# Optimization experiments

Hardware: AMD Instinct MI355X
Metric: run time of the kernel (lower is better)

Reference implementation:

```python
import jax, jax.numpy as jnp
import numpy as np

N_USERS = 100000
N_ITEMS = 50000
N = N_USERS + N_ITEMS
EMB_DIM = 64
N_LAYERS = 3
NNZ = 6400000
BATCH = 4096


def setup_inputs() -> dict:
    key = jax.random.key(0)
    k = jax.random.split(key, 7)
    user_emb = 0.1 * jax.random.normal(k[0], (N_USERS, EMB_DIM), dtype=jnp.float32)
    item_emb = 0.1 * jax.random.normal(k[1], (N_ITEMS, EMB_DIM), dtype=jnp.float32)
    graph_val = jax.random.uniform(k[2], (NNZ,), dtype=jnp.float32) * 0.05
    graph_src = jax.random.randint(k[3], (NNZ,), 0, N, dtype=jnp.int64) if jax.config.jax_enable_x64 else jax.random.randint(k[3], (NNZ,), 0, N).astype(jnp.int32)
    graph_dst = jax.random.randint(k[4], (NNZ,), 0, N).astype(graph_src.dtype)
    users = jax.random.randint(k[5], (BATCH,), 0, N_USERS).astype(graph_src.dtype)
    items = jax.random.randint(k[6], (BATCH,), 0, N_ITEMS).astype(graph_src.dtype)
    return {"user_emb": user_emb, "item_emb": item_emb, "graph_val": graph_val,
            "graph_src": graph_src, "graph_dst": graph_dst, "users": users, "items": items}


def _spmm(val, src, dst, x):
    # y[src] += val * x[dst]  -- sparse (COO) matrix @ dense
    return jax.ops.segment_sum(val[:, None] * x[dst], src, num_segments=N)


def reference(user_emb, item_emb, graph_val, graph_src, graph_dst, users, items):
    all_emb = jnp.concatenate([user_emb, item_emb], axis=0)  # [N, d]
    acc = all_emb  # running sum over layers (fused mean accumulation)
    x = all_emb
    for _ in range(N_LAYERS):
        x = _spmm(graph_val, graph_src, graph_dst, x)
        acc = acc + x
    light_out = acc / (N_LAYERS + 1)
    all_users = light_out[:N_USERS]
    all_items = light_out[N_USERS:]
    scores = jnp.sum(all_users[users] * all_items[items], axis=1)  # [B]
    return scores
```

## Files before the change

### kernel.cpp

```cpp
#include <hip/hip_runtime.h>


constexpr int N_USERS = 100000;
constexpr int N_ITEMS = 50000;
constexpr int N_NODES = N_USERS + N_ITEMS;
constexpr int EMB = 64;
constexpr int NNZ = 6400000;
constexpr int BATCH = 4096;

constexpr int BSHIFT = 9;
constexpr int BWIDTH = 1 << BSHIFT;
constexpr int NB = (N_NODES + BWIDTH - 1) >> BSHIFT;
constexpr int NBPAD = 512;
constexpr int BSTRIDE = 23500;
constexpr int PBSTRIDE = 26624;

constexpr int TILE = 5120;
constexpr int P1_BLOCKS = NNZ / TILE;
constexpr int EPT1 = TILE / 256;

constexpr float QSCALE = 327680.0f;
constexpr float QINV   = 1.0f / 327680.0f;

__global__ void gcur_init_kernel(int* __restrict__ gcur) {
    int i = blockIdx.x * blockDim.x + threadIdx.x;
    if (i < NB) gcur[i] = i * BSTRIDE;
}

__global__ void p1_bin_kernel(const int* __restrict__ src, const int* __restrict__ dst,
                              const float* __restrict__ val, int* __restrict__ gcur,
                              uint2* __restrict__ staging) {
    __shared__ int hist[NBPAD];
    __shared__ int gbase[NBPAD];
    __shared__ int cur[NBPAD];
    __shared__ int sbuf[NBPAD];
    __shared__ int lbase[NBPAD];
    __shared__ uint2 ebuf[TILE];
    int t = threadIdx.x;
    int tile = blockIdx.x * TILE;
    int srcs[EPT1];
    #pragma unroll
    for (int k = 0; k < EPT1; ++k) srcs[k] = src[tile + t + k * 256];
    for (int i = t; i < NBPAD; i += 256) { hist[i] = 0; cur[i] = 0; }
    __syncthreads();
    #pragma unroll
    for (int k = 0; k < EPT1; ++k) atomicAdd(&hist[srcs[k] >> BSHIFT], 1);
    __syncthreads();
    for (int i = t; i < NB; i += 256) {
        int h = hist[i];
        gbase[i] = (h > 0) ? atomicAdd(&gcur[i], h) : 0;
    }
    for (int i = t; i < NBPAD; i += 256) sbuf[i] = hist[i];
    __syncthreads();
    int* pin = sbuf; int* pout = lbase;
    for (int off = 1; off < NBPAD; off <<= 1) {
        for (int i = t; i < NBPAD; i += 256) {
            int v = pin[i];
            if (i >= off) v += pin[i - off];
            pout[i] = v;
        }
        __syncthreads();
        int* tmp = pin; pin = pout; pout = tmp;
    }
    for (int i = t; i < NBPAD; i += 256) lbase[i] = pin[i] - hist[i];
    __syncthreads();
    #pragma unroll
    for (int k = 0; k < EPT1; ++k) {
        int i = tile + t + k * 256;
        int s = srcs[k];
        int b = s >> BSHIFT;
        int c = atomicAdd(&cur[b], 1);
        int d = dst[i];
        float v = val[i];
        unsigned q = (unsigned)(v * QSCALE);
        if (q > 16383u) q = 16383u;
        ebuf[lbase[b] + c] = make_uint2((q << 18) | (unsigned)d, (unsigned)s);
    }
    __syncthreads();
    #pragma unroll
    for (int k = 0; k < EPT1; ++k) {
        int j = t + k * 256;
        uint2 e = ebuf[j];
        int b = (int)(e.y >> BSHIFT);
        unsigned pos = (unsigned)(gbase[b] + (j - lbase[b]));
        if (pos < (unsigned)((b + 1) * BSTRIDE))
            staging[pos] = e;
    }
}

__global__ void p2_sort_kernel(const int* __restrict__ gcur, const uint2* __restrict__ staging,
                               unsigned* __restrict__ epack, unsigned* __restrict__ prow) {
    __shared__ int hist[BWIDTH], sA[BWIDTH], sB[BWIDTH], cur[BWIDTH];
    int b = blockIdx.x;
    int t = threadIdx.x;
    int cnt = gcur[b] - b * BSTRIDE;
    if (cnt > BSTRIDE) cnt = BSTRIDE;
    int sbase = b * BSTRIDE;
    hist[t] = 0;
    __syncthreads();
    for (int j = t; j < cnt; j += 512) {
        uint2 e = staging[sbase + j];
        atomicAdd(&hist[e.y & (BWIDTH - 1)], 1);
    }
    __syncthreads();
    sA[t] = (hist[t] + 7) >> 3;
    __syncthreads();
    int* pin = sA; int* pout = sB;
    for (int off = 1; off < BWIDTH; off <<= 1) {
        int v = pin[t];
        if (t >= off) v += pin[t - off];
        pout[t] = v;
        __syncthreads();
        int* tmp = pin; pin = pout; pout = tmp;
    }
    {
        int c = hist[t];
        int pw = (c + 7) >> 3;
        int ps = pin[t] - pw;
        unsigned poff = (unsigned)(b * PBSTRIDE + 8 * ps);
        int fit = (PBSTRIDE - 8 * ps) >> 3;
        if (fit < 0) fit = 0;
        if (pw > fit) pw = fit;
        if (pw > 15) pw = 15;
        cur[t] = (int)poff;
        int node = (b << BSHIFT) + t;
        if (node < N_NODES) prow[node] = (poff << 4) | (unsigned)pw;
        for (int s = c; s < 8 * pw; ++s) epack[poff + s] = 0;
    }
    __syncthreads();
    unsigned bend = (unsigned)((b + 1) * PBSTRIDE);
    for (int j = t; j < cnt; j += 512) {
        uint2 e = staging[sbase + j];
        int p = atomicAdd(&cur[e.y & (BWIDTH - 1)], 1);
        if ((unsigned)p < bend) epack[p] = e.x;
    }
}

__device__ __forceinline__ float ubf0(unsigned x) { return (float)(x & 0xffu); }
__device__ __forceinline__ float ubf1(unsigned x) { return (float)((x >> 8) & 0xffu); }
__device__ __forceinline__ float ubf2(unsigned x) { return (float)((x >> 16) & 0xffu); }
__device__ __forceinline__ float ubf3(unsigned x) { return (float)(x >> 24); }

__global__ void initq_kernel(const float* __restrict__ ue, const float* __restrict__ ie,
                             unsigned char* __restrict__ x8, float* __restrict__ scl) {
    int gid = blockIdx.x * blockDim.x + threadIdx.x;
    int row = gid >> 3;
    if (row >= N_NODES) return;
    int l8 = threadIdx.x & 7;
    const float* srcp = (row < N_USERS) ? (ue + (size_t)row * EMB)
                                        : (ie + (size_t)(row - N_USERS) * EMB);
    const float4* p = (const float4*)(srcp + l8 * 8);
    float4 f0 = p[0], f1 = p[1];
    float v[8] = {f0.x, f0.y, f0.z, f0.w, f1.x, f1.y, f1.z, f1.w};
    float m = 0.f;
    #pragma unroll
    for (int k = 0; k < 8; ++k) m = fmaxf(m, fabsf(v[k]));
    m = fmaxf(m, __shfl_xor(m, 1, 64));
    m = fmaxf(m, __shfl_xor(m, 2, 64));
    m = fmaxf(m, __shfl_xor(m, 4, 64));
    float inv = (m > 0.f) ? 127.f / m : 0.f;
    unsigned w0 = 0, w1 = 0;
    #pragma unroll
    for (int k = 0; k < 4; ++k)
        w0 |= (((unsigned)((int)rintf(v[k] * inv) + 128)) & 0xffu) << (8 * k);
    #pragma unroll
    for (int k = 0; k < 4; ++k)
        w1 |= (((unsigned)((int)rintf(v[4 + k] * inv) + 128)) & 0xffu) << (8 * k);
    *(uint2*)(x8 + (((size_t)row) << 6) + l8 * 8) = make_uint2(w0, w1);
    if (l8 == 0) scl[row] = m * (1.f / 127.f);
}

__global__ void gather_init_kernel(const float* __restrict__ ue, const float* __restrict__ ie,
                                   const int* __restrict__ users, const int* __restrict__ items,
                                   float* __restrict__ accb) {
    int gid = blockIdx.x * blockDim.x + threadIdx.x;
    int w = gid >> 6;
    int lane = threadIdx.x & 63;
    if (w >= BATCH * 2) return;
    int b = w >> 1;
    float v;
    if (w & 1) v = ie[(long long)items[b] * EMB + lane];
    else       v = ue[(long long)users[b] * EMB + lane];
    accb[(long long)w * EMB + lane] = v;
}

__global__ void gather_addq_kernel(const unsigned char* __restrict__ x8,
                                   const float* __restrict__ scl,
                                   const int* __restrict__ users, const int* __restrict__ items,
                                   float* __restrict__ accb) {
    int gid = blockIdx.x * blockDim.x + threadIdx.x;
    int w = gid >> 6;
    int lane = threadIdx.x & 63;
    if (w >= BATCH * 2) return;
    int b = w >> 1;
    int node = (w & 1) ? (N_USERS + items[b]) : users[b];
    float s = scl[node];
    float xv = s * ((float)x8[(((size_t)node) << 6) + lane] - 128.f);
    accb[(long long)w * EMB + lane] += xv;
}

__device__ __forceinline__ void row_gather_q8(unsigned pr, int lane,
                                              const unsigned* __restrict__ epack,
                                              const unsigned char* __restrict__ x8,
                                              const float* __restrict__ scl,
                                              float acc[8]) {
    const int l8 = lane & 7;
    const int qb = lane & 56;
    const unsigned li8 = (unsigned)l8 * 8u;
    float a0 = 0, a1 = 0, a2 = 0, a3 = 0, a4 = 0, a5 = 0, a6 = 0, a7 = 0;
    float b0 = 0, b1 = 0, b2 = 0, b3 = 0, b4 = 0, b5 = 0, b6 = 0, b7 = 0;
    float S = 0.f;
    const unsigned* ep = epack + (pr >> 4);
    int nwin = (int)(pr & 15u);
    if (nwin > 0) {
        unsigned e = ep[l8];
        for (int w = 0; w < nwin; ++w) {
            unsigned en = ep[8 + l8];
            ep += 8;
            unsigned d = e & 0x3FFFFu;
            float v = ((float)(e >> 18) + 0.5f) * QINV;
            float vs = v * scl[d];
            unsigned voff = d << 6;
            #pragma unroll
            for (int t = 0; t < 8; t += 2) {
                unsigned offA = (unsigned)__shfl((int)voff, qb + t, 64);
                unsigned offB = (unsigned)__shfl((int)voff, qb + t + 1, 64);
                float vA = __shfl(vs, qb + t, 64);
                float vB = __shfl(vs, qb + t + 1, 64);
                uint2 pa = *(const uint2*)(x8 + (offA | li8));
                uint2 pb = *(const uint2*)(x8 + (offB | li8));
                a0 += vA * ubf0(pa.x);  a1 += vA * ubf1(pa.x);
                a2 += vA * ubf2(pa.x);  a3 += vA * ubf3(pa.x);
                a4 += vA * ubf0(pa.y);  a5 += vA * ubf1(pa.y);
                a6 += vA * ubf2(pa.y);  a7 += vA * ubf3(pa.y);
                b0 += vB * ubf0(pb.x);  b1 += vB * ubf1(pb.x);
                b2 += vB * ubf2(pb.x);  b3 += vB * ubf3(pb.x);
                b4 += vB * ubf0(pb.y);  b5 += vB * ubf1(pb.y);
                b6 += vB * ubf2(pb.y);  b7 += vB * ubf3(pb.y);
                S += vA + vB;
            }
            e = en;
        }
    }
    float c = 128.f * S;
    acc[0] = a0 + b0 - c; acc[1] = a1 + b1 - c; acc[2] = a2 + b2 - c;
    acc[3] = a3 + b3 - c; acc[4] = a4 + b4 - c; acc[5] = a5 + b5 - c;
    acc[6] = a6 + b6 - c; acc[7] = a7 + b7 - c;
}

__global__ void spmmq_kernel(const unsigned* __restrict__ prow,
                             const unsigned* __restrict__ epack,
                             const unsigned char* __restrict__ x8,
                             const float* __restrict__ sclin,
                             unsigned char* __restrict__ y8,
                             float* __restrict__ sclout) {
    int gid = blockIdx.x * blockDim.x + threadIdx.x;
    int row = gid >> 3;
    if (row >= N_NODES) return;
    int lane = threadIdx.x & 63;
    float acc[8];
    row_gather_q8(prow[row], lane, epack, x8, sclin, acc);
    float m = 0.f;
    #pragma unroll
    for (int k = 0; k < 8; ++k) m = fmaxf(m, fabsf(acc[k]));
    m = fmaxf(m, __shfl_xor(m, 1, 64));
    m = fmaxf(m, __shfl_xor(m, 2, 64));
    m = fmaxf(m, __shfl_xor(m, 4, 64));
    float inv = (m > 0.f) ? 127.f / m : 0.f;
    unsigned w0 = 0, w1 = 0;
    #pragma unroll
    for (int k = 0; k < 4; ++k)
        w0 |= (((unsigned)((int)rintf(acc[k] * inv) + 128)) & 0xffu) << (8 * k);
    #pragma unroll
    for (int k = 0; k < 4; ++k)
        w1 |= (((unsigned)((int)rintf(acc[4 + k] * inv) + 128)) & 0xffu) << (8 * k);
    int l8 = lane & 7;
    *(uint2*)(y8 + (((size_t)row) << 6) + l8 * 8) = make_uint2(w0, w1);
    if (l8 == 0) sclout[row] = m * (1.f / 127.f);
}

__global__ void spmm_selq_kernel(const unsigned* __restrict__ prow,
                                 const unsigned* __restrict__ epack,
                                 const unsigned char* __restrict__ x8,
                                 const float* __restrict__ scl,
                                 const int* __restrict__ users, const int* __restrict__ items,
                                 float* __restrict__ accb) {
    int gid = blockIdx.x * blockDim.x + threadIdx.x;
    int g = gid >> 3;
    if (g >= BATCH * 2) return;
    int lane = threadIdx.x & 63;
    int b = g >> 1;
    int node = (g & 1) ? (N_USERS + items[b]) : users[b];
    float acc[8];
    row_gather_q8(prow[node], lane, epack, x8, scl, acc);
    float4* p = (float4*)(accb + ((long long)g << 6) + (lane & 7) * 8);
    float4 c0 = p[0], c1 = p[1];
    c0.x += acc[0]; c0.y += acc[1]; c0.z += acc[2]; c0.w += acc[3];
    c1.x += acc[4]; c1.y += acc[5]; c1.z += acc[6]; c1.w += acc[7];
    p[0] = c0; p[1] = c1;
}

__global__ void score_kernel(const float* __restrict__ accb, float* __restrict__ out) {
    int gid = blockIdx.x * blockDim.x + threadIdx.x;
    int b = gid >> 6;
    int lane = threadIdx.x & 63;
    if (b >= BATCH) return;
    float a = accb[(long long)(2 * b) * EMB + lane];
    float c = accb[(long long)(2 * b + 1) * EMB + lane];
    float p = a * c;
    #pragma unroll
    for (int off = 32; off > 0; off >>= 1) p += __shfl_down(p, off, 64);
    if (lane == 0) out[b] = p * (1.0f / 16.0f);
}

extern "C" void kernel_launch(void* const* d_in, const int* in_sizes, int n_in,
                              void* d_out, int out_size, void* d_ws, size_t ws_size,
                              hipStream_t stream) {
    const float* user_emb  = (const float*)d_in[0];
    const float* item_emb  = (const float*)d_in[1];
    const float* graph_val = (const float*)d_in[2];
    const int*   graph_src = (const int*)d_in[3];
    const int*   graph_dst = (const int*)d_in[4];
    const int*   users     = (const int*)d_in[5];
    const int*   items     = (const int*)d_in[6];
    float* out = (float*)d_out;

    char* base = (char*)d_ws;
    const size_t STAGE_BYTES = (size_t)BSTRIDE * NB * 8;
    const size_t XQBYTES = (size_t)N_NODES * 64;
    const size_t ACCB_BYTES = (size_t)BATCH * 2 * EMB * 4;
    const size_t PB_SLOTS = (size_t)PBSTRIDE * NB;
    uint2*         staging = (uint2*)base;
    unsigned char* A8      = (unsigned char*)base;
    unsigned char* B8      = A8 + XQBYTES;
    float*         accb    = (float*)(base + 2 * XQBYTES);
    float*         scA     = (float*)(base + 2 * XQBYTES + ACCB_BYTES);
    float*         scB     = scA + N_NODES;
    unsigned*      epack   = (unsigned*)(base + STAGE_BYTES);
    unsigned*      prow    = epack + PB_SLOTS;
    int*           gcur    = (int*)(prow + N_NODES);

    const int wblocks = (BATCH * 2 * 64) / 256;
    const int sblocks = (N_NODES * 8 + 255) / 256;
    const int selblocks = (BATCH * 2 * 8) / 256;

    gcur_init_kernel<<<(NB + 255) / 256, 256, 0, stream>>>(gcur);
    p1_bin_kernel<<<P1_BLOCKS, 256, 0, stream>>>(graph_src, graph_dst, graph_val,
                                                 gcur, staging);
    p2_sort_kernel<<<NB, 512, 0, stream>>>(gcur, staging, epack, prow);

    initq_kernel<<<sblocks, 256, 0, stream>>>(user_emb, item_emb, A8, scA);
    gather_init_kernel<<<wblocks, 256, 0, stream>>>(user_emb, item_emb, users, items, accb);

    spmmq_kernel<<<sblocks, 256, 0, stream>>>(prow, epack, A8, scA, B8, scB);
    gather_addq_kernel<<<wblocks, 256, 0, stream>>>(B8, scB, users, items, accb);

    spmmq_kernel<<<sblocks, 256, 0, stream>>>(prow, epack, B8, scB, A8, scA);
    gather_addq_kernel<<<wblocks, 256, 0, stream>>>(A8, scA, users, items, accb);

    spmm_selq_kernel<<<selblocks, 256, 0, stream>>>(prow, epack, A8, scA, users, items, accb);

    score_kernel<<<(BATCH * 64) / 256, 256, 0, stream>>>(accb, out);
}
```

Measured before the change: 489.3 us.

## Horizontally fuse build, quantize and gather kernels; add nontemporal memory hints

Merges edge binning, initial int8 quantization and the batch gather-init into one launch using block-index ranges. Each gather-add is folded into the following SpMM launch, and the last gather-add is merged with the selective final SpMM, using atomics on the batch accumulator. The sort kernel now runs 1024 threads per block, and nontemporal loads and stores are applied to streaming edge and embedding traffic. The workspace layout is reorganised so that staging aliases the second quantized buffer. Together these cut launch count and let independent work overlap, at the cost of atomics and more complex kernels.

Result: slower. 603.4 us (+23.3%).

```diff
diff --git a/kernel.cpp b/kernel.cpp
--- a/kernel.cpp
+++ b/kernel.cpp
@@ -18,73 +18,140 @@
 constexpr int TILE = 5120;
 constexpr int P1_BLOCKS = NNZ / TILE;
 constexpr int EPT1 = TILE / 256;
+constexpr int IQ_BLOCKS = (N_NODES * 8 + 255) / 256;
+constexpr int GI_BLOCKS = (BATCH * 2 * 64) / 256;
+constexpr int SBLOCKS  = (N_NODES * 8 + 255) / 256;
+constexpr int SELBLOCKS = (BATCH * 2 * 8) / 256;
 
 constexpr float QSCALE = 327680.0f;
 constexpr float QINV   = 1.0f / 327680.0f;
+
+__device__ __forceinline__ unsigned ntl_u32(const unsigned* p) { return __builtin_nontemporal_load(p); }
+__device__ __forceinline__ int      ntl_i32(const int* p)      { return __builtin_nontemporal_load(p); }
+__device__ __forceinline__ float    ntl_f32(const float* p)    { return __builtin_nontemporal_load(p); }
+__device__ __forceinline__ unsigned long long ntl_u64(const unsigned long long* p) { return __builtin_nontemporal_load(p); }
+__device__ __forceinline__ void nts_u32(unsigned v, unsigned* p) { __builtin_nontemporal_store(v, p); }
+__device__ __forceinline__ void nts_u64(unsigned long long v, unsigned long long* p) { __builtin_nontemporal_store(v, p); }
 
 __global__ void gcur_init_kernel(int* __restrict__ gcur) {
     int i = blockIdx.x * blockDim.x + threadIdx.x;
     if (i < NB) gcur[i] = i * BSTRIDE;
 }
 
-__global__ void p1_bin_kernel(const int* __restrict__ src, const int* __restrict__ dst,
-                              const float* __restrict__ val, int* __restrict__ gcur,
-                              uint2* __restrict__ staging) {
-    __shared__ int hist[NBPAD];
-    __shared__ int gbase[NBPAD];
-    __shared__ int cur[NBPAD];
-    __shared__ int sbuf[NBPAD];
-    __shared__ int lbase[NBPAD];
-    __shared__ uint2 ebuf[TILE];
+__device__ __forceinline__ float ubf0(unsigned x) { return (float)(x & 0xffu); }
+__device__ __forceinline__ float ubf1(unsigned x) { return (float)((x >> 8) & 0xffu); }
+__device__ __forceinline__ float ubf2(unsigned x) { return (float)((x >> 16) & 0xffu); }
+__device__ __forceinline__ float ubf3(unsigned x) { return (float)(x >> 24); }
+
+__global__ void fused_build_kernel(const int* __restrict__ src, const int* __restrict__ dst,
+                                   const float* __restrict__ val, int* __restrict__ gcur,
+                                   uint2* __restrict__ staging,
+                                   const float* __restrict__ ue, const float* __restrict__ ie,
+                                   const int* __restrict__ users, const int* __restrict__ items,
+                                   unsigned char* __restrict__ x8, float* __restrict__ scl,
+                                   float* __restrict__ accb) {
+    int bx = blockIdx.x;
     int t = threadIdx.x;
-    int tile = blockIdx.x * TILE;
-    int srcs[EPT1];
-    #pragma unroll
-    for (int k = 0; k < EPT1; ++k) srcs[k] = src[tile + t + k * 256];
-    for (int i = t; i < NBPAD; i += 256) { hist[i] = 0; cur[i] = 0; }
-    __syncthreads();
-    #pragma unroll
-    for (int k = 0; k < EPT1; ++k) atomicAdd(&hist[srcs[k] >> BSHIFT], 1);
-    __syncthreads();
-    for (int i = t; i < NB; i += 256) {
-        int h = hist[i];
-        gbase[i] = (h > 0) ? atomicAdd(&gcur[i], h) : 0;
-    }
-    for (int i = t; i < NBPAD; i += 256) sbuf[i] = hist[i];
-    __syncthreads();
-    int* pin = sbuf; int* pout = lbase;
-    for (int off = 1; off < NBPAD; off <<= 1) {
-        for (int i = t; i < NBPAD; i += 256) {
-            int v = pin[i];
-            if (i >= off) v += pin[i - off];
-            pout[i] = v;
-        }
-        __syncthreads();
-        int* tmp = pin; pin = pout; pout = tmp;
-    }
-    for (int i = t; i < NBPAD; i += 256) lbase[i] = pin[i] - hist[i];
-    __syncthreads();
-    #pragma unroll
-    for (int k = 0; k < EPT1; ++k) {
-        int i = tile + t + k * 256;
-        int s = srcs[k];
-        int b = s >> BSHIFT;
-        int c = atomicAdd(&cur[b], 1);
-        int d = dst[i];
-        float v = val[i];
-        unsigned q = (unsigned)(v * QSCALE);
-        if (q > 16383u) q = 16383u;
-        ebuf[lbase[b] + c] = make_uint2((q << 18) | (unsigned)d, (unsigned)s);
-    }
-    __syncthreads();
-    #pragma unroll
-    for (int k = 0; k < EPT1; ++k) {
-        int j = t + k * 256;
-        uint2 e = ebuf[j];
-        int b = (int)(e.y >> BSHIFT);
-        unsigned pos = (unsigned)(gbase[b] + (j - lbase[b]));
-        if (pos < (unsigned)((b + 1) * BSTRIDE))
-            staging[pos] = e;
+    if (bx < P1_BLOCKS) {
+        __shared__ int hist[NBPAD];
+        __shared__ int gbase[NBPAD];
+        __shared__ int cur[NBPAD];
+        __shared__ int sbuf[NBPAD];
+        __shared__ int lbase[NBPAD];
+        __shared__ uint2 ebuf[TILE];
+        int tile = bx * TILE;
+        int srcs[EPT1];
+        #pragma unroll
+        for (int k = 0; k < EPT1; ++k) srcs[k] = ntl_i32(src + tile + t + k * 256);
+        for (int i = t; i < NBPAD; i += 256) { hist[i] = 0; cur[i] = 0; }
+        __syncthreads();
+        #pragma unroll
+        for (int k = 0; k < EPT1; ++k) atomicAdd(&hist[srcs[k] >> BSHIFT], 1);
+        __syncthreads();
+        for (int i = t; i < NB; i += 256) {
+            int h = hist[i];
+            gbase[i] = (h > 0) ? atomicAdd(&gcur[i], h) : 0;
+        }
+        for (int i = t; i < NBPAD; i += 256) sbuf[i] = hist[i];
+        __syncthreads();
+        int* pin = sbuf; int* pout = lbase;
+        for (int off = 1; off < NBPAD; off <<= 1) {
+            for (int i = t; i < NBPAD; i += 256) {
+                int v = pin[i];
+                if (i >= off) v += pin[i - off];
+                pout[i] = v;
+            }
+            __syncthreads();
+            int* tmp = pin; pin = pout; pout = tmp;
+        }
+        for (int i = t; i < NBPAD; i += 256) lbase[i] = pin[i] - hist[i];
+        __syncthreads();
+        #pragma unroll
+        for (int k = 0; k < EPT1; ++k) {
+            int i = tile + t + k * 256;
+            int s = srcs[k];
+            int b = s >> BSHIFT;
+            int c = atomicAdd(&cur[b], 1);
+            int d = ntl_i32(dst + i);
+            float v = ntl_f32(val + i);
+            unsigned q = (unsigned)(v * QSCALE);
+            if (q > 16383u) q = 16383u;
+            ebuf[lbase[b] + c] = make_uint2((q << 18) | (unsigned)d, (unsigned)s);
+        }
+        __syncthreads();
+        #pragma unroll
+        for (int k = 0; k < EPT1; ++k) {
+            int j = t + k * 256;
+            uint2 e = ebuf[j];
+            int b = (int)(e.y >> BSHIFT);
+            unsigned pos = (unsigned)(gbase[b] + (j - lbase[b]));
+            if (pos < (unsigned)((b + 1) * BSTRIDE))
+                nts_u64(((unsigned long long)e.y << 32) | (unsigned long long)e.x,
+                        (unsigned long long*)&staging[pos]);
+        }
+        return;
+    }
+    bx -= P1_BLOCKS;
+    if (bx < IQ_BLOCKS) {
+        int gid = bx * 256 + t;
+        int row = gid >> 3;
+        if (row >= N_NODES) return;
+        int l8 = t & 7;
+        const float* srcp = (row < N_USERS) ? (ue + (size_t)row * EMB)
+                                            : (ie + (size_t)(row - N_USERS) * EMB);
+        const float4* p = (const float4*)(srcp + l8 * 8);
+        float4 f0 = p[0], f1 = p[1];
+        float v[8] = {f0.x, f0.y, f0.z, f0.w, f1.x, f1.y, f1.z, f1.w};
+        float m = 0.f;
+        #pragma unroll
+        for (int k = 0; k < 8; ++k) m = fmaxf(m, fabsf(v[k]));
+        m = fmaxf(m, __shfl_xor(m, 1, 64));
+        m = fmaxf(m, __shfl_xor(m, 2, 64));
+        m = fmaxf(m, __shfl_xor(m, 4, 64));
+        float inv = (m > 0.f) ? 127.f / m : 0.f;
+        unsigned w0 = 0, w1 = 0;
+        #pragma unroll
+        for (int k = 0; k < 4; ++k)
+            w0 |= (((unsigned)((int)rintf(v[k] * inv) + 128)) & 0xffu) << (8 * k);
+        #pragma unroll
+        for (int k = 0; k < 4; ++k)
+            w1 |= (((unsigned)((int)rintf(v[4 + k] * inv) + 128)) & 0xffu) << (8 * k);
+        nts_u64(((unsigned long long)w1 << 32) | (unsigned long long)w0,
+                (unsigned long long*)(x8 + (((size_t)row) << 6) + l8 * 8));
+        if (l8 == 0) scl[row] = m * (1.f / 127.f);
+        return;
+    }
+    bx -= IQ_BLOCKS;
+    {
+        int gid = bx * 256 + t;
+        int w = gid >> 6;
+        int lane = t & 63;
+        if (w >= BATCH * 2) return;
+        int b = w >> 1;
+        float v;
+        if (w & 1) v = ie[(long long)items[b] * EMB + lane];
+        else       v = ue[(long long)users[b] * EMB + lane];
+        accb[(long long)w * EMB + lane] = v;
     }
 }
 
@@ -95,25 +162,28 @@
     int t = threadIdx.x;
     int cnt = gcur[b] - b * BSTRIDE;
     if (cnt > BSTRIDE) cnt = BSTRIDE;
+    if (cnt < 0) cnt = 0;
     int sbase = b * BSTRIDE;
-    hist[t] = 0;
+    if (t < BWIDTH) hist[t] = 0;
     __syncthreads();
-    for (int j = t; j < cnt; j += 512) {
+    for (int j = t; j < cnt; j += 1024) {
         uint2 e = staging[sbase + j];
         atomicAdd(&hist[e.y & (BWIDTH - 1)], 1);
     }
     __syncthreads();
-    sA[t] = (hist[t] + 7) >> 3;
+    if (t < BWIDTH) sA[t] = (hist[t] + 7) >> 3;
     __syncthreads();
     int* pin = sA; int* pout = sB;
     for (int off = 1; off < BWIDTH; off <<= 1) {
-        int v = pin[t];
-        if (t >= off) v += pin[t - off];
-        pout[t] = v;
+        if (t < BWIDTH) {
+            int v = pin[t];
+            if (t >= off) v += pin[t - off];
+            pout[t] = v;
+        }
         __syncthreads();
         int* tmp = pin; pin = pout; pout = tmp;
     }
-    {
+    if (t < BWIDTH) {
         int c = hist[t];
         int pw = (c + 7) >> 3;
         int ps = pin[t] - pw;
@@ -129,74 +199,13 @@
     }
     __syncthreads();
     unsigned bend = (unsigned)((b + 1) * PBSTRIDE);
-    for (int j = t; j < cnt; j += 512) {
-        uint2 e = staging[sbase + j];
-        int p = atomicAdd(&cur[e.y & (BWIDTH - 1)], 1);
-        if ((unsigned)p < bend) epack[p] = e.x;
-    }
-}
-
-__device__ __forceinline__ float ubf0(unsigned x) { return (float)(x & 0xffu); }
-__device__ __forceinline__ float ubf1(unsigned x) { return (float)((x >> 8) & 0xffu); }
-__device__ __forceinline__ float ubf2(unsigned x) { return (float)((x >> 16) & 0xffu); }
-__device__ __forceinline__ float ubf3(unsigned x) { return (float)(x >> 24); }
-
-__global__ void initq_kernel(const float* __restrict__ ue, const float* __restrict__ ie,
-                             unsigned char* __restrict__ x8, float* __restrict__ scl) {
-    int gid = blockIdx.x * blockDim.x + threadIdx.x;
-    int row = gid >> 3;
-    if (row >= N_NODES) return;
-    int l8 = threadIdx.x & 7;
-    const float* srcp = (row < N_USERS) ? (ue + (size_t)row * EMB)
-                                        : (ie + (size_t)(row - N_USERS) * EMB);
-    const float4* p = (const float4*)(srcp + l8 * 8);
-    float4 f0 = p[0], f1 = p[1];
-    float v[8] = {f0.x, f0.y, f0.z, f0.w, f1.x, f1.y, f1.z, f1.w};
-    float m = 0.f;
-    #pragma unroll
-    for (int k = 0; k < 8; ++k) m = fmaxf(m, fabsf(v[k]));
-    m = fmaxf(m, __shfl_xor(m, 1, 64));
-    m = fmaxf(m, __shfl_xor(m, 2, 64));
-    m = fmaxf(m, __shfl_xor(m, 4, 64));
-    float inv = (m > 0.f) ? 127.f / m : 0.f;
-    unsigned w0 = 0, w1 = 0;
-    #pragma unroll
-    for (int k = 0; k < 4; ++k)
-        w0 |= (((unsigned)((int)rintf(v[k] * inv) + 128)) & 0xffu) << (8 * k);
-    #pragma unroll
-    for (int k = 0; k < 4; ++k)
-        w1 |= (((unsigned)((int)rintf(v[4 + k] * inv) + 128)) & 0xffu) << (8 * k);
-    *(uint2*)(x8 + (((size_t)row) << 6) + l8 * 8) = make_uint2(w0, w1);
-    if (l8 == 0) scl[row] = m * (1.f / 127.f);
-}
-
-__global__ void gather_init_kernel(const float* __restrict__ ue, const float* __restrict__ ie,
-                                   const int* __restrict__ users, const int* __restrict__ items,
-                                   float* __restrict__ accb) {
-    int gid = blockIdx.x * blockDim.x + threadIdx.x;
-    int w = gid >> 6;
-    int lane = threadIdx.x & 63;
-    if (w >= BATCH * 2) return;
-    int b = w >> 1;
-    float v;
-    if (w & 1) v = ie[(long long)items[b] * EMB + lane];
-    else       v = ue[(long long)users[b] * EMB + lane];
-    accb[(long long)w * EMB + lane] = v;
-}
-
-__global__ void gather_addq_kernel(const unsigned char* __restrict__ x8,
-                                   const float* __restrict__ scl,
-                                   const int* __restrict__ users, const int* __restrict__ items,
-                                   float* __restrict__ accb) {
-    int gid = blockIdx.x * blockDim.x + threadIdx.x;
-    int w = gid >> 6;
-    int lane = threadIdx.x & 63;
-    if (w >= BATCH * 2) return;
-    int b = w >> 1;
-    int node = (w & 1) ? (N_USERS + items[b]) : users[b];
-    float s = scl[node];
-    float xv = s * ((float)x8[(((size_t)node) << 6) + lane] - 128.f);
-    accb[(long long)w * EMB + lane] += xv;
+    for (int j = t; j < cnt; j += 1024) {
+        unsigned long long ev = ntl_u64((const unsigned long long*)&staging[sbase + j]);
+        unsigned ex = (unsigned)ev;
+        int row = (int)((ev >> 32) & (unsigned long long)(BWIDTH - 1));
+        int p = atomicAdd(&cur[row], 1);
+        if ((unsigned)p < bend) nts_u32(ex, &epack[p]);
+    }
 }
 
 __device__ __forceinline__ void row_gather_q8(unsigned pr, int lane,
@@ -213,9 +222,9 @@
     const unsigned* ep = epack + (pr >> 4);
     int nwin = (int)(pr & 15u);
     if (nwin > 0) {
-        unsigned e = ep[l8];
+        unsigned e = ntl_u32(ep + l8);
         for (int w = 0; w < nwin; ++w) {
-            unsigned en = ep[8 + l8];
+            unsigned en = ntl_u32(ep + 8 + l8);
             ep += 8;
             unsigned d = e & 0x3FFFFu;
             float v = ((float)(e >> 18) + 0.5f) * QINV;
@@ -248,56 +257,93 @@
     acc[6] = a6 + b6 - c; acc[7] = a7 + b7 - c;
 }
 
-__global__ void spmmq_kernel(const unsigned* __restrict__ prow,
-                             const unsigned* __restrict__ epack,
-                             const unsigned char* __restrict__ x8,
-                             const float* __restrict__ sclin,
-                             unsigned char* __restrict__ y8,
-                             float* __restrict__ sclout) {
-    int gid = blockIdx.x * blockDim.x + threadIdx.x;
-    int row = gid >> 3;
-    if (row >= N_NODES) return;
-    int lane = threadIdx.x & 63;
-    float acc[8];
-    row_gather_q8(prow[row], lane, epack, x8, sclin, acc);
-    float m = 0.f;
-    #pragma unroll
-    for (int k = 0; k < 8; ++k) m = fmaxf(m, fabsf(acc[k]));
-    m = fmaxf(m, __shfl_xor(m, 1, 64));
-    m = fmaxf(m, __shfl_xor(m, 2, 64));
-    m = fmaxf(m, __shfl_xor(m, 4, 64));
-    float inv = (m > 0.f) ? 127.f / m : 0.f;
-    unsigned w0 = 0, w1 = 0;
-    #pragma unroll
-    for (int k = 0; k < 4; ++k)
-        w0 |= (((unsigned)((int)rintf(acc[k] * inv) + 128)) & 0xffu) << (8 * k);
-    #pragma unroll
-    for (int k = 0; k < 4; ++k)
-        w1 |= (((unsigned)((int)rintf(acc[4 + k] * inv) + 128)) & 0xffu) << (8 * k);
-    int l8 = lane & 7;
-    *(uint2*)(y8 + (((size_t)row) << 6) + l8 * 8) = make_uint2(w0, w1);
-    if (l8 == 0) sclout[row] = m * (1.f / 127.f);
-}
-
-__global__ void spmm_selq_kernel(const unsigned* __restrict__ prow,
-                                 const unsigned* __restrict__ epack,
-                                 const unsigned char* __restrict__ x8,
-                                 const float* __restrict__ scl,
-                                 const int* __restrict__ users, const int* __restrict__ items,
-                                 float* __restrict__ accb) {
-    int gid = blockIdx.x * blockDim.x + threadIdx.x;
-    int g = gid >> 3;
-    if (g >= BATCH * 2) return;
-    int lane = threadIdx.x & 63;
-    int b = g >> 1;
-    int node = (g & 1) ? (N_USERS + items[b]) : users[b];
-    float acc[8];
-    row_gather_q8(prow[node], lane, epack, x8, scl, acc);
-    float4* p = (float4*)(accb + ((long long)g << 6) + (lane & 7) * 8);
-    float4 c0 = p[0], c1 = p[1];
-    c0.x += acc[0]; c0.y += acc[1]; c0.z += acc[2]; c0.w += acc[3];
-    c1.x += acc[4]; c1.y += acc[5]; c1.z += acc[6]; c1.w += acc[7];
-    p[0] = c0; p[1] = c1;
+__global__ void spmmq_fused_kernel(const unsigned* __restrict__ prow,
+                                   const unsigned* __restrict__ epack,
+                                   const unsigned char* __restrict__ x8in,
+                                   const float* __restrict__ sclin,
+                                   unsigned char* __restrict__ y8,
+                                   float* __restrict__ sclout,
+                                   const int* __restrict__ users,
+                                   const int* __restrict__ items,
+                                   float* __restrict__ accb) {
+    int bx = blockIdx.x;
+    int t = threadIdx.x;
+    if (bx < SBLOCKS) {
+        int gid = bx * 256 + t;
+        int row = gid >> 3;
+        if (row >= N_NODES) return;
+        int lane = t & 63;
+        unsigned pr = ntl_u32(prow + row);
+        float acc[8];
+        row_gather_q8(pr, lane, epack, x8in, sclin, acc);
+        float m = 0.f;
+        #pragma unroll
+        for (int k = 0; k < 8; ++k) m = fmaxf(m, fabsf(acc[k]));
+        m = fmaxf(m, __shfl_xor(m, 1, 64));
+        m = fmaxf(m, __shfl_xor(m, 2, 64));
+        m = fmaxf(m, __shfl_xor(m, 4, 64));
+        float inv = (m > 0.f) ? 127.f / m : 0.f;
+        unsigned w0 = 0, w1 = 0;
+        #pragma unroll
+        for (int k = 0; k < 4; ++k)
+            w0 |= (((unsigned)((int)rintf(acc[k] * inv) + 128)) & 0xffu) << (8 * k);
+        #pragma unroll
+        for (int k = 0; k < 4; ++k)
+            w1 |= (((unsigned)((int)rintf(acc[4 + k] * inv) + 128)) & 0xffu) << (8 * k);
+        int l8 = lane & 7;
+        nts_u64(((unsigned long long)w1 << 32) | (unsigned long long)w0,
+                (unsigned long long*)(y8 + (((size_t)row) << 6) + l8 * 8));
+        if (l8 == 0) sclout[row] = m * (1.f / 127.f);
+        return;
+    }
+    bx -= SBLOCKS;
+    {
+        int gid = bx * 256 + t;
+        int w = gid >> 6;
+        int lane = t & 63;
+        if (w >= BATCH * 2) return;
+        int b = w >> 1;
+        int node = (w & 1) ? (N_USERS + items[b]) : users[b];
+        float s = sclin[node];
+        float xv = s * ((float)x8in[(((size_t)node) << 6) + lane] - 128.f);
+        accb[(long long)w * EMB + lane] += xv;
+    }
+}
+
+__global__ void tail_kernel(const unsigned* __restrict__ prow,
+                            const unsigned* __restrict__ epack,
+                            const unsigned char* __restrict__ x8,
+                            const float* __restrict__ scl,
+                            const int* __restrict__ users, const int* __restrict__ items,
+                            float* __restrict__ accb) {
+    int bx = blockIdx.x;
+    int t = threadIdx.x;
+    if (bx < GI_BLOCKS) {
+        int gid = bx * 256 + t;
+        int w = gid >> 6;
+        int lane = t & 63;
+        if (w >= BATCH * 2) return;
+        int b = w >> 1;
+        int node = (w & 1) ? (N_USERS + items[b]) : users[b];
+        float s = scl[node];
+        float xv = s * ((float)x8[(((size_t)node) << 6) + lane] - 128.f);
+        atomicAdd(&accb[(long long)w * EMB + lane], xv);
+        return;
+    }
+    bx -= GI_BLOCKS;
+    {
+        int gid = bx * 256 + t;
+        int g = gid >> 3;
+        if (g >= BATCH * 2) return;
+        int lane = t & 63;
+        int b = g >> 1;
+        int node = (g & 1) ? (N_USERS + items[b]) : users[b];
+        float acc[8];
+        row_gather_q8(ntl_u32(prow + node), lane, epack, x8, scl, acc);
+        float* p = accb + ((long long)g << 6) + (lane & 7) * 8;
+        #pragma unroll
+        for (int k = 0; k < 8; ++k) atomicAdd(p + k, acc[k]);
+    }
 }
 
 __global__ void score_kernel(const float* __restrict__ accb, float* __restrict__ out) {
@@ -340,25 +386,36 @@
     unsigned*      prow    = epack + PB_SLOTS;
     int*           gcur    = (int*)(prow + N_NODES);
 
-    const int wblocks = (BATCH * 2 * 64) / 256;
-    const int sblocks = (N_NODES * 8 + 255) / 256;
-    const int selblocks = (BATCH * 2 * 8) / 256;
+    const size_t X_REGION = 2 * XQBYTES + ACCB_BYTES + 2 * (size_t)N_NODES * 4;
+    const size_t X_REGION_AL = (X_REGION + 255) & ~(size_t)255;
+    staging = (uint2*)(base + X_REGION_AL);
+    epack   = (unsigned*)(base + X_REGION_AL + STAGE_BYTES);
+    prow    = epack + PB_SLOTS;
+    gcur    = (int*)(prow + N_NODES);
+    accb = (float*)(gcur + 512);
+    scA  = accb + (size_t)BATCH * 2 * EMB;
+    scB  = scA + N_NODES;
+    A8   = (unsigned char*)base;
+    B8   = A8 + XQBYTES;
+    staging = (uint2*)(base + XQBYTES);
+    epack   = (unsigned*)(base + XQBYTES + STAGE_BYTES);
+    prow    = epack + PB_SLOTS;
+    gcur    = (int*)(prow + N_NODES);
+    accb    = (float*)(gcur + 512);
+    scA     = accb + (size_t)BATCH * 2 * EMB;
+    scB     = scA + N_NODES;
 
     gcur_init_kernel<<<(NB + 255) / 256, 256, 0, stream>>>(gcur);
-    p1_bin_kernel<<<P1_BLOCKS, 256, 0, stream>>>(graph_src, graph_dst, graph_val,
-                                                 gcur, staging);
-    p2_sort_kernel<<<NB, 512, 0, stream>>>(gcur, staging, epack, prow);
-
-    initq_kernel<<<sblocks, 256, 0, stream>>>(user_emb, item_emb, A8, scA);
-    gather_init_kernel<<<wblocks, 256, 0, stream>>>(user_emb, item_emb, users, items, accb);
-
-    spmmq_kernel<<<sblocks, 256, 0, stream>>>(prow, epack, A8, scA, B8, scB);
-    gather_addq_kernel<<<wblocks, 256, 0, stream>>>(B8, scB, users, items, accb);
-
-    spmmq_kernel<<<sblocks, 256, 0, stream>>>(prow, epack, B8, scB, A8, scA);
-    gather_addq_kernel<<<wblocks, 256, 0, stream>>>(A8, scA, users, items, accb);
-
-    spmm_selq_kernel<<<selblocks, 256, 0, stream>>>(prow, epack, A8, scA, users, items, accb);
-
+    fused_build_kernel<<<P1_BLOCKS + IQ_BLOCKS + GI_BLOCKS, 256, 0, stream>>>(
+        graph_src, graph_dst, graph_val, gcur, staging,
+        user_emb, item_emb, users, items, A8, scA, accb);
+    p2_sort_kernel<<<NB, 1024, 0, stream>>>(gcur, staging, epack, prow);
+
+    spmmq_fused_kernel<<<SBLOCKS, 256, 0, stream>>>(prow, epack, A8, scA, B8, scB,
+                                                    users, items, accb);
+    spmmq_fused_kernel<<<SBLOCKS + GI_BLOCKS, 256, 0, stream>>>(prow, epack, B8, scB,
+                                                                A8, scA, users, items, accb);
+    tail_kernel<<<GI_BLOCKS + SELBLOCKS, 256, 0, stream>>>(prow, epack, A8, scA,
+                                                           users, items, accb);
     score_kernel<<<(BATCH * 64) / 256, 256, 0, stream>>>(accb, out);
 }
```
